# Performance work log

Measured on AMD Instinct MI355X. Metric: run time of the kernel, lower is better.

## Reference

```python
import jax, jax.numpy as jnp
import numpy as np

VOCAB = 10000
N_NODES = 50000
D = 256
N_TYPES = 3
N_LAYERS = 4
E_PER_TYPE = 300000


def setup_inputs() -> dict:
    key = jax.random.key(0)
    k1, k2, k3, k4 = jax.random.split(key, 4)
    node_label_ids = jax.random.randint(k1, (N_NODES,), 0, VOCAB)
    adjacency_lists = jax.random.randint(k2, (N_TYPES, E_PER_TYPE, 2), 0, N_NODES)
    emb_table = jax.random.normal(k3, (VOCAB, D), dtype=jnp.float32)
    # scale ~ glorot so 4 relu layers don't blow up
    layer_weights = jax.random.normal(k4, (N_LAYERS, N_TYPES, D, D), dtype=jnp.float32) / jnp.sqrt(jnp.float32(D))
    return {
        "node_label_ids": node_label_ids,
        "adjacency_lists": adjacency_lists,
        "emb_table": emb_table,
        "layer_weights": layer_weights,
    }


def reference(node_label_ids, adjacency_lists, emb_table, layer_weights):
    n_nodes = node_label_ids.shape[0]
    # embedding lookup (node label -> initial node state); emb dim == hidden dim
    h = emb_table[node_label_ids]  # [N, D]
    n_layers, n_types = layer_weights.shape[0], layer_weights.shape[1]
    for l in range(n_layers):
        agg = jnp.zeros_like(h)
        for t in range(n_types):
            src = adjacency_lists[t, :, 0]
            tgt = adjacency_lists[t, :, 1]
            # gather source states, per-edge-type linear message transform
            msg = h[src] @ layer_weights[l, t]  # [E, D]
            # scatter-sum messages onto target nodes
            agg = agg + jax.ops.segment_sum(msg, tgt, num_segments=n_nodes)
        h = jax.nn.relu(agg)
    return h
```

## Files before the change

### kernel.cpp

```cpp
#include <hip/hip_runtime.h>

#define NN 50000
#define DD 256
#define NT 3
#define NL 4
#define EPT 300000
#define KK 768
#define SCAN_BLOCKS 196
#define MROWS 50048

typedef __attribute__((ext_vector_type(8))) short bf16x8;
typedef __attribute__((ext_vector_type(4))) float f32x4;
typedef __attribute__((ext_vector_type(4))) unsigned int u32x4;

__device__ __forceinline__ unsigned short f2bf(float f) {
  unsigned u = __builtin_bit_cast(unsigned, f);
  unsigned r = u + 0x7fffu + ((u >> 16) & 1u);
  return (unsigned short)(r >> 16);
}
__device__ __forceinline__ float bflo2f(unsigned u) {
  return __builtin_bit_cast(float, u << 16);
}
__device__ __forceinline__ float bfhi2f(unsigned u) {
  return __builtin_bit_cast(float, u & 0xffff0000u);
}

__global__ void gather_emb(const int* __restrict__ labels,
                           const float* __restrict__ emb,
                           unsigned short* __restrict__ h) {
  int node = blockIdx.x;
  int lane = threadIdx.x;
  float4 v = ((const float4*)(emb + (size_t)labels[node] * DD))[lane];
  unsigned a = (unsigned)f2bf(v.x) | ((unsigned)f2bf(v.y) << 16);
  unsigned b = (unsigned)f2bf(v.z) | ((unsigned)f2bf(v.w) << 16);
  ((uint2*)(h + (size_t)node * DD))[lane] = make_uint2(a, b);
}

__global__ void zero_kernel(float* __restrict__ p, int n4) {
  int i = blockIdx.x * blockDim.x + threadIdx.x;
  int stride = gridDim.x * blockDim.x;
  float4* p4 = (float4*)p;
  for (; i < n4; i += stride) p4[i] = make_float4(0.f, 0.f, 0.f, 0.f);
}

__global__ __launch_bounds__(256) void wconv(const float* __restrict__ Wl,
                                             unsigned short* __restrict__ WT) {
  int i = blockIdx.x * 256 + threadIdx.x;
  int l = i / (DD * KK);
  int rem = i % (DD * KK);
  int n = rem / KK;
  int kk = rem % KK;
  int t = kk >> 8;
  int k = kk & 255;
  float v = Wl[((size_t)(l * NT + t) * DD + k) * DD + n];
  WT[i] = f2bf(v);
}

__global__ __launch_bounds__(256) void hist_kernel(const int* __restrict__ adj,
                                                   int* __restrict__ counts) {
  int t = blockIdx.y;
  int e = blockIdx.x * 256 + threadIdx.x;
  if (e >= EPT) return;
  int tgt = adj[(size_t)t * EPT * 2 + 2 * e + 1];
  atomicAdd(&counts[t * NN + tgt], 1);
}

__global__ __launch_bounds__(256) void scan1(const int* __restrict__ counts,
                                             int* __restrict__ rowptr,
                                             int* __restrict__ bsums) {
  int t = blockIdx.y, b = blockIdx.x;
  int i = b * 256 + threadIdx.x;
  int v = (i < NN) ? counts[t * NN + i] : 0;
  __shared__ int s[256];
  s[threadIdx.x] = v;
  __syncthreads();
  for (int off = 1; off < 256; off <<= 1) {
    int y = (threadIdx.x >= off) ? s[threadIdx.x - off] : 0;
    __syncthreads();
    s[threadIdx.x] += y;
    __syncthreads();
  }
  if (i < NN) rowptr[t * (NN + 1) + i] = s[threadIdx.x] - v;
  if (threadIdx.x == 255) bsums[t * SCAN_BLOCKS + b] = s[255];
}

__global__ __launch_bounds__(256) void scan2(int* __restrict__ bsums) {
  int t = blockIdx.x;
  int v = (threadIdx.x < SCAN_BLOCKS) ? bsums[t * SCAN_BLOCKS + threadIdx.x] : 0;
  __shared__ int s[256];
  s[threadIdx.x] = v;
  __syncthreads();
  for (int off = 1; off < 256; off <<= 1) {
    int y = (threadIdx.x >= off) ? s[threadIdx.x - off] : 0;
    __syncthreads();
    s[threadIdx.x] += y;
    __syncthreads();
  }
  if (threadIdx.x < SCAN_BLOCKS) bsums[t * SCAN_BLOCKS + threadIdx.x] = s[threadIdx.x] - v;
}

__global__ __launch_bounds__(256) void scan3(int* __restrict__ rowptr,
                                             const int* __restrict__ bsums,
                                             int* __restrict__ cursor) {
  int t = blockIdx.y, b = blockIdx.x;
  int i = b * 256 + threadIdx.x;
  if (i < NN) {
    int r = rowptr[t * (NN + 1) + i] + bsums[t * SCAN_BLOCKS + b];
    rowptr[t * (NN + 1) + i] = r;
    cursor[t * NN + i] = r;
  }
  if (b == 0 && threadIdx.x == 0) rowptr[t * (NN + 1) + NN] = EPT;
}

__global__ __launch_bounds__(256) void bucket_kernel(const int* __restrict__ adj,
                                                     int* __restrict__ cursor,
                                                     int* __restrict__ esrc) {
  int t = blockIdx.y;
  int e = blockIdx.x * 256 + threadIdx.x;
  if (e >= EPT) return;
  int s = adj[(size_t)t * EPT * 2 + 2 * e];
  int tgt = adj[(size_t)t * EPT * 2 + 2 * e + 1];
  int pos = atomicAdd(&cursor[t * NN + tgt], 1);
  esrc[(size_t)t * EPT + pos] = s;
}

__global__ __launch_bounds__(256) void agg_csr(const int* __restrict__ rowptr,
                                               const int* __restrict__ esrc,
                                               const unsigned short* __restrict__ h,
                                               unsigned short* __restrict__ Gcat) {
  int t = blockIdx.y;
  int node = blockIdx.x * 8 + (threadIdx.x >> 5);
  if (node >= NN) return;
  int sub = threadIdx.x & 31;
  const int* rp = rowptr + t * (NN + 1);
  const int* es = esrc + (size_t)t * EPT;
  int e = rp[node];
  int end = rp[node + 1];
  const u32x4* h4 = (const u32x4*)h;
  float a0 = 0.f, a1 = 0.f, a2 = 0.f, a3 = 0.f, a4 = 0.f, a5 = 0.f, a6 = 0.f, a7 = 0.f;
  for (; e + 3 < end; e += 4) {
    u32x4 v0 = h4[(size_t)es[e] * 32 + sub];
    u32x4 v1 = h4[(size_t)es[e + 1] * 32 + sub];
    u32x4 v2 = h4[(size_t)es[e + 2] * 32 + sub];
    u32x4 v3 = h4[(size_t)es[e + 3] * 32 + sub];
    a0 += (bflo2f(v0.x) + bflo2f(v1.x)) + (bflo2f(v2.x) + bflo2f(v3.x));
    a1 += (bfhi2f(v0.x) + bfhi2f(v1.x)) + (bfhi2f(v2.x) + bfhi2f(v3.x));
    a2 += (bflo2f(v0.y) + bflo2f(v1.y)) + (bflo2f(v2.y) + bflo2f(v3.y));
    a3 += (bfhi2f(v0.y) + bfhi2f(v1.y)) + (bfhi2f(v2.y) + bfhi2f(v3.y));
    a4 += (bflo2f(v0.z) + bflo2f(v1.z)) + (bflo2f(v2.z) + bflo2f(v3.z));
    a5 += (bfhi2f(v0.z) + bfhi2f(v1.z)) + (bfhi2f(v2.z) + bfhi2f(v3.z));
    a6 += (bflo2f(v0.w) + bflo2f(v1.w)) + (bflo2f(v2.w) + bflo2f(v3.w));
    a7 += (bfhi2f(v0.w) + bfhi2f(v1.w)) + (bfhi2f(v2.w) + bfhi2f(v3.w));
  }
  for (; e < end; ++e) {
    u32x4 v0 = h4[(size_t)es[e] * 32 + sub];
    a0 += bflo2f(v0.x);
    a1 += bfhi2f(v0.x);
    a2 += bflo2f(v0.y);
    a3 += bfhi2f(v0.y);
    a4 += bflo2f(v0.z);
    a5 += bfhi2f(v0.z);
    a6 += bflo2f(v0.w);
    a7 += bfhi2f(v0.w);
  }
  u32x4 o;
  o.x = (unsigned)f2bf(a0) | ((unsigned)f2bf(a1) << 16);
  o.y = (unsigned)f2bf(a2) | ((unsigned)f2bf(a3) << 16);
  o.z = (unsigned)f2bf(a4) | ((unsigned)f2bf(a5) << 16);
  o.w = (unsigned)f2bf(a6) | ((unsigned)f2bf(a7) << 16);
  ((u32x4*)(Gcat + (size_t)node * KK + t * DD))[sub] = o;
}

template <int OUTF32>
__global__ __launch_bounds__(256) void gemm_bf16(const unsigned short* __restrict__ A,
                                                 const unsigned short* __restrict__ BT,
                                                 void* __restrict__ Cout) {
  __shared__ __align__(16) char lds[32768];
  const int tid = threadIdx.x;
  const int w = tid >> 6, lane = tid & 63;
  const int m0 = blockIdx.x * 128;
  const int n0 = blockIdx.y * 128;
  const int wm = (w >> 1) * 64, wn = (w & 1) * 64;
  const int r15 = lane & 15;
  const int g16 = (lane >> 4) * 16;

  f32x4 acc[4][4] = {};
  const char* Ab = (const char*)A;
  const char* Bb = (const char*)BT;

  const int srow = tid >> 1;
  const int scol0 = (tid & 1) * 64;
  const int ssw = (srow & 7) << 4;
  u32x4 ra[4], rb[4];

  const int NTK = KK / 64;

#define GLOAD(kt)                                                          \
  {                                                                        \
    const char* ap = Ab + (size_t)(m0 + srow) * (KK * 2) + (size_t)(kt)*128; \
    const char* bp = Bb + (size_t)(n0 + srow) * (KK * 2) + (size_t)(kt)*128; \
    _Pragma("unroll") for (int p = 0; p < 4; p++) {                        \
      ra[p] = *(const u32x4*)(ap + scol0 + p * 16);                        \
      rb[p] = *(const u32x4*)(bp + scol0 + p * 16);                        \
    }                                                                      \
  }
#define SWRITE()                                                           \
  {                                                                        \
    _Pragma("unroll") for (int p = 0; p < 4; p++) {                        \
      int sc = (scol0 + p * 16) ^ ssw;                                     \
      *(u32x4*)(lds + srow * 128 + sc) = ra[p];                            \
      *(u32x4*)(lds + 16384 + srow * 128 + sc) = rb[p];                    \
    }                                                                      \
  }

  GLOAD(0);
  SWRITE();
  __syncthreads();
  for (int kt = 0; kt < NTK; ++kt) {
    if (kt + 1 < NTK) GLOAD(kt + 1);
#pragma unroll
    for (int ks = 0; ks < 2; ++ks) {
      bf16x8 af[4], bfr[4];
#pragma unroll
      for (int mf = 0; mf < 4; ++mf) {
        int row = wm + mf * 16 + r15;
        af[mf] = *(const bf16x8*)(lds + row * 128 + ((ks * 64 + g16) ^ ((row & 7) << 4)));
      }
#pragma unroll
      for (int nf = 0; nf < 4; ++nf) {
        int row = wn + nf * 16 + r15;
        bfr[nf] = *(const bf16x8*)(lds + 16384 + row * 128 + ((ks * 64 + g16) ^ ((row & 7) << 4)));
      }
#pragma unroll
      for (int mf = 0; mf < 4; ++mf)
#pragma unroll
        for (int nf = 0; nf < 4; ++nf)
          acc[mf][nf] =
              __builtin_amdgcn_mfma_f32_16x16x32_bf16(af[mf], bfr[nf], acc[mf][nf], 0, 0, 0);
    }
    if (kt + 1 < NTK) {
      __syncthreads();
      SWRITE();
      __syncthreads();
    }
  }

#pragma unroll
  for (int mf = 0; mf < 4; ++mf) {
#pragma unroll
    for (int r = 0; r < 4; ++r) {
      int grow = m0 + wm + mf * 16 + (lane >> 4) * 4 + r;
      if (grow >= NN) continue;
#pragma unroll
      for (int nf = 0; nf < 4; ++nf) {
        int gcol = n0 + wn + nf * 16 + r15;
        float v = fmaxf(acc[mf][nf][r], 0.f);
        if (OUTF32)
          ((float*)Cout)[(size_t)grow * DD + gcol] = v;
        else
          ((unsigned short*)Cout)[(size_t)grow * DD + gcol] = f2bf(v);
      }
    }
  }
#undef GLOAD
#undef SWRITE
}

extern "C" void kernel_launch(void* const* d_in, const int* in_sizes, int n_in,
                              void* d_out, int out_size, void* d_ws, size_t ws_size,
                              hipStream_t stream) {
  const int* labels = (const int*)d_in[0];
  const int* adj = (const int*)d_in[1];
  const float* emb = (const float*)d_in[2];
  const float* Wl = (const float*)d_in[3];

  char* base = (char*)d_ws;
  unsigned short* h = (unsigned short*)base;
  size_t off = (size_t)NN * DD * 2;
  unsigned short* Gcat = (unsigned short*)(base + off);
  off += (size_t)MROWS * KK * 2;
  unsigned short* WT = (unsigned short*)(base + off);
  off += (size_t)NL * DD * KK * 2;
  int* rowptr = (int*)(base + off);
  off += (size_t)((NT * (NN + 1) * 4 + 15) & ~15);
  int* esrc = (int*)(base + off);

  int* counts = (int*)Gcat;
  int* cursor = (int*)((char*)Gcat + (1 << 20));
  int* bsums = (int*)((char*)Gcat + (2 << 20));

  wconv<<<(NL * DD * KK) / 256, 256, 0, stream>>>(Wl, WT);
  gather_emb<<<NN, 64, 0, stream>>>(labels, emb, h);

  zero_kernel<<<256, 256, 0, stream>>>((float*)counts, (3 * NN) / 4);
  {
    dim3 g((EPT + 255) / 256, NT);
    hist_kernel<<<g, 256, 0, stream>>>(adj, counts);
  }
  {
    dim3 g(SCAN_BLOCKS, NT);
    scan1<<<g, 256, 0, stream>>>(counts, rowptr, bsums);
  }
  scan2<<<NT, 256, 0, stream>>>(bsums);
  {
    dim3 g(SCAN_BLOCKS, NT);
    scan3<<<g, 256, 0, stream>>>(rowptr, bsums, cursor);
  }
  {
    dim3 g((EPT + 255) / 256, NT);
    bucket_kernel<<<g, 256, 0, stream>>>(adj, cursor, esrc);
  }

  dim3 ga((NN + 7) / 8, NT);
  dim3 gg(MROWS / 128, 2);
  for (int l = 0; l < NL; ++l) {
    agg_csr<<<ga, 256, 0, stream>>>(rowptr, esrc, h, Gcat);
    const unsigned short* WTl = WT + (size_t)l * DD * KK;
    if (l < NL - 1)
      gemm_bf16<0><<<gg, 256, 0, stream>>>(Gcat, WTl, h);
    else
      gemm_bf16<1><<<gg, 256, 0, stream>>>(Gcat, WTl, d_out);
  }
}
```

Before: 580.6 us.

## Widen GEMM block tile to cover full output width with 512 threads

The bf16 GEMM now has each 512-thread block compute a 128x256 output tile covering the full hidden width, replacing 256-thread 128x128 tiles on a 2D grid. Each block loads its A (aggregated features) tile once instead of twice across the two N-blocks, which cuts global reads of the large activation matrix. In exchange, LDS use per block rises to 48KB and the grid shrinks to about 391 blocks, which may lower occupancy and load balance on the GPU.

```diff
diff --git a/kernel.cpp b/kernel.cpp
--- a/kernel.cpp
+++ b/kernel.cpp
@@ -172,15 +172,14 @@
 }
 
 template <int OUTF32>
-__global__ __launch_bounds__(256) void gemm_bf16(const unsigned short* __restrict__ A,
+__global__ __launch_bounds__(512) void gemm_bf16(const unsigned short* __restrict__ A,
                                                  const unsigned short* __restrict__ BT,
                                                  void* __restrict__ Cout) {
-  __shared__ __align__(16) char lds[32768];
+  __shared__ __align__(16) char lds[49152];
   const int tid = threadIdx.x;
   const int w = tid >> 6, lane = tid & 63;
   const int m0 = blockIdx.x * 128;
-  const int n0 = blockIdx.y * 128;
-  const int wm = (w >> 1) * 64, wn = (w & 1) * 64;
+  const int wm = (w >> 2) * 64, wn = (w & 3) * 64;
   const int r15 = lane & 15;
   const int g16 = (lane >> 4) * 16;
 
@@ -188,29 +187,31 @@
   const char* Ab = (const char*)A;
   const char* Bb = (const char*)BT;
 
-  const int srow = tid >> 1;
-  const int scol0 = (tid & 1) * 64;
-  const int ssw = (srow & 7) << 4;
-  u32x4 ra[4], rb[4];
+  const int arow = tid >> 2;
+  const int acol = (tid & 3) * 32;
+  const int asw = (arow & 7) << 4;
+  const int brow = tid >> 1;
+  const int bcol = (tid & 1) * 64;
+  const int bsw = (brow & 7) << 4;
+  u32x4 ra[2], rb[4];
 
   const int NTK = KK / 64;
 
-#define GLOAD(kt)                                                          \
-  {                                                                        \
-    const char* ap = Ab + (size_t)(m0 + srow) * (KK * 2) + (size_t)(kt)*128; \
-    const char* bp = Bb + (size_t)(n0 + srow) * (KK * 2) + (size_t)(kt)*128; \
-    _Pragma("unroll") for (int p = 0; p < 4; p++) {                        \
-      ra[p] = *(const u32x4*)(ap + scol0 + p * 16);                        \
-      rb[p] = *(const u32x4*)(bp + scol0 + p * 16);                        \
-    }                                                                      \
-  }
-#define SWRITE()                                                           \
-  {                                                                        \
-    _Pragma("unroll") for (int p = 0; p < 4; p++) {                        \
-      int sc = (scol0 + p * 16) ^ ssw;                                     \
-      *(u32x4*)(lds + srow * 128 + sc) = ra[p];                            \
-      *(u32x4*)(lds + 16384 + srow * 128 + sc) = rb[p];                    \
-    }                                                                      \
+#define GLOAD(kt)                                                            \
+  {                                                                          \
+    const char* ap = Ab + (size_t)(m0 + arow) * (KK * 2) + (size_t)(kt)*128; \
+    const char* bp = Bb + (size_t)brow * (KK * 2) + (size_t)(kt)*128;        \
+    ra[0] = *(const u32x4*)(ap + acol);                                      \
+    ra[1] = *(const u32x4*)(ap + acol + 16);                                 \
+    _Pragma("unroll") for (int p = 0; p < 4; p++) rb[p] =                    \
+        *(const u32x4*)(bp + bcol + p * 16);                                 \
+  }
+#define SWRITE()                                                             \
+  {                                                                          \
+    *(u32x4*)(lds + arow * 128 + (acol ^ asw)) = ra[0];                      \
+    *(u32x4*)(lds + arow * 128 + ((acol + 16) ^ asw)) = ra[1];               \
+    _Pragma("unroll") for (int p = 0; p < 4; p++) *(u32x4*)(                 \
+        lds + 16384 + brow * 128 + ((bcol + p * 16) ^ bsw)) = rb[p];         \
   }
 
   GLOAD(0);
@@ -229,7 +230,8 @@
 #pragma unroll
       for (int nf = 0; nf < 4; ++nf) {
         int row = wn + nf * 16 + r15;
-        bfr[nf] = *(const bf16x8*)(lds + 16384 + row * 128 + ((ks * 64 + g16) ^ ((row & 7) << 4)));
+        bfr[nf] =
+            *(const bf16x8*)(lds + 16384 + row * 128 + ((ks * 64 + g16) ^ ((row & 7) << 4)));
       }
 #pragma unroll
       for (int mf = 0; mf < 4; ++mf)
@@ -253,7 +255,7 @@
       if (grow >= NN) continue;
 #pragma unroll
       for (int nf = 0; nf < 4; ++nf) {
-        int gcol = n0 + wn + nf * 16 + r15;
+        int gcol = wn + nf * 16 + r15;
         float v = fmaxf(acc[mf][nf][r], 0.f);
         if (OUTF32)
           ((float*)Cout)[(size_t)grow * DD + gcol] = v;
@@ -312,13 +314,13 @@
   }
 
   dim3 ga((NN + 7) / 8, NT);
-  dim3 gg(MROWS / 128, 2);
+  const int gg = MROWS / 128;
   for (int l = 0; l < NL; ++l) {
     agg_csr<<<ga, 256, 0, stream>>>(rowptr, esrc, h, Gcat);
     const unsigned short* WTl = WT + (size_t)l * DD * KK;
     if (l < NL - 1)
-      gemm_bf16<0><<<gg, 256, 0, stream>>>(Gcat, WTl, h);
+      gemm_bf16<0><<<gg, 512, 0, stream>>>(Gcat, WTl, h);
     else
-      gemm_bf16<1><<<gg, 256, 0, stream>>>(Gcat, WTl, d_out);
-  }
-}
+      gemm_bf16<1><<<gg, 512, 0, stream>>>(Gcat, WTl, d_out);
+  }
+}
```

Result: faster. 519.6 us (-10.5%).
